# Kernel optimization log

Measured on AMD Instinct MI355X. Metric: run time of the kernel, lower is better.

Reference implementation:

```python
import jax, jax.numpy as jnp
import numpy as np

B, T, I, H = 64, 512, 512, 512

def setup_inputs() -> dict:
    key = jax.random.key(0)
    ks = jax.random.split(key, 13)
    s = 0.02
    return {
        'inputs': jax.random.normal(ks[0], (B, T, I), dtype=jnp.float32),
        'W_i': jax.random.normal(ks[1], (I, H), dtype=jnp.float32) * s,
        'W_f': jax.random.normal(ks[2], (I, H), dtype=jnp.float32) * s,
        'W_o': jax.random.normal(ks[3], (I, H), dtype=jnp.float32) * s,
        'W_c': jax.random.normal(ks[4], (I, H), dtype=jnp.float32) * s,
        'U_i': jax.random.normal(ks[5], (H, H), dtype=jnp.float32) * s,
        'U_f': jax.random.normal(ks[6], (H, H), dtype=jnp.float32) * s,
        'U_o': jax.random.normal(ks[7], (H, H), dtype=jnp.float32) * s,
        'U_c': jax.random.normal(ks[8], (H, H), dtype=jnp.float32) * s,
        'b_i': jax.random.normal(ks[9], (1, H), dtype=jnp.float32) * s,
        'b_f': jax.random.normal(ks[10], (1, H), dtype=jnp.float32) * s,
        'b_o': jax.random.normal(ks[11], (1, H), dtype=jnp.float32) * s,
        'b_c': jax.random.normal(ks[12], (1, H), dtype=jnp.float32) * s,
    }

def reference(inputs, W_i, W_f, W_o, W_c, U_i, U_f, U_o, U_c, b_i, b_f, b_o, b_c):
    batch = inputs.shape[0]
    hidden = U_i.shape[0]
    # Precompute input projections for all 4 gates in one fused GEMM: [T, B, 4H]
    W = jnp.concatenate([W_i, W_f, W_o, W_c], axis=1)          # [I, 4H]
    b = jnp.concatenate([b_i, b_f, b_o, b_c], axis=1)          # [1, 4H]
    U = jnp.concatenate([U_i, U_f, U_o, U_c], axis=1)          # [H, 4H]
    x_proj = jnp.einsum('bti,ig->tbg', inputs, W) + b          # [T, B, 4H]

    def step(carry, xg):
        h, c = carry
        g = xg + h @ U                                          # [B, 4H]
        i_g = jax.nn.sigmoid(g[:, 0*hidden:1*hidden])
        f_g = jax.nn.sigmoid(g[:, 1*hidden:2*hidden])
        o_g = jax.nn.sigmoid(g[:, 2*hidden:3*hidden])
        c_t = jnp.tanh(g[:, 3*hidden:4*hidden])
        c = f_g * c + i_g * c_t
        h = o_g * jnp.tanh(c)
        return (h, c), None

    h0 = jnp.zeros((batch, hidden), dtype=inputs.dtype)
    c0 = jnp.zeros((batch, hidden), dtype=inputs.dtype)
    (h, c), _ = jax.lax.scan(step, (h0, c0), x_proj)
    return h
```

## Files before the change

kernel.cpp:

```cpp
#include <hip/hip_runtime.h>
#include <hip/hip_bf16.h>
#include <cstdint>


typedef __bf16 bf16;
typedef __bf16 bf16x8 __attribute__((ext_vector_type(8)));
typedef float floatx4 __attribute__((ext_vector_type(4)));
typedef uint64_t u64;
typedef uint32_t u32;

#define T_STEPS 512

#define XP_OFF     0ull
#define XBF_OFF    134217728ull
#define WCT_OFF    167772160ull
#define USW_OFF    169869312ull
#define BCAT_OFF   171966464ull
#define HBUF_OFF   171974656ull

__device__ inline u32 pack_bf16x2(float a, float b) {
    union { __bf16 h[2]; u32 u; } cv;
    cv.h[0] = (__bf16)a; cv.h[1] = (__bf16)b;
    return cv.u;
}
__device__ inline float bf_lo(u32 w) { return __builtin_bit_cast(float, w << 16); }
__device__ inline float bf_hi(u32 w) { return __builtin_bit_cast(float, w & 0xffff0000u); }

__global__ void k0a_convert(const float* __restrict__ in, bf16* __restrict__ xbf) {
    int o = blockIdx.x * 256 + threadIdx.x;
    int k = o & 511;
    int r = o >> 9;
    int t = r >> 6, b = r & 63;
    xbf[o] = (bf16)in[(b * 512 + t) * 512 + k];
}

__global__ void k0b_wcat(const float* __restrict__ Wi, const float* __restrict__ Wf,
                         const float* __restrict__ Wo, const float* __restrict__ Wc,
                         const float* __restrict__ bi, const float* __restrict__ bfv,
                         const float* __restrict__ bo, const float* __restrict__ bc,
                         bf16* __restrict__ wct, float* __restrict__ bcat) {
    int o = blockIdx.x * 256 + threadIdx.x;
    int k = o & 511;
    int c = o >> 9;
    int h = c >> 2, g = c & 3;
    const float* W = (g == 0) ? Wi : (g == 1) ? Wf : (g == 2) ? Wo : Wc;
    wct[o] = (bf16)W[k * 512 + h];
    if (o < 2048) {
        int hh = o >> 2, gg = o & 3;
        const float* bv = (gg == 0) ? bi : (gg == 1) ? bfv : (gg == 2) ? bo : bc;
        bcat[o] = bv[hh];
    }
}

__global__ void k0c_uswz(const float* __restrict__ Ui, const float* __restrict__ Uf,
                         const float* __restrict__ Uo, const float* __restrict__ Uc,
                         bf16* __restrict__ usw) {
    int o = blockIdx.x * 256 + threadIdx.x;
    int e  = o & 7;
    int l  = (o >> 3) & 63;
    int ks = (o >> 9) & 15;
    int nt = (o >> 13) & 1;
    int w  = (o >> 14) & 3;
    int s  = o >> 16;
    int k = ks * 32 + (l >> 4) * 8 + e;
    int col_local = (2 * w + nt) * 16 + (l & 15);
    int h = s * 32 + (col_local >> 2);
    int g = col_local & 3;
    const float* U = (g == 0) ? Ui : (g == 1) ? Uf : (g == 2) ? Uo : Uc;
    usw[o] = (bf16)U[k * 512 + h];
}

__launch_bounds__(256, 2)
__global__ void k1_gemm(const bf16* __restrict__ xbf, const bf16* __restrict__ wct,
                        const float* __restrict__ bcat, bf16* __restrict__ xp) {
    __shared__ bf16 As[128 * 40];
    __shared__ bf16 Bs[128 * 40];
    int tid = threadIdx.x;
    int wid = tid >> 6, lane = tid & 63;
    int q = lane >> 4, m = lane & 15;
    int wr = wid >> 1, wc = wid & 1;
    int br = blockIdx.x & 255, bc = blockIdx.x >> 8;

    floatx4 acc[4][4] = {};

    for (int kk = 0; kk < 16; ++kk) {
        #pragma unroll
        for (int cc = 0; cc < 2; ++cc) {
            int ch = tid + cc * 256;
            int row = ch >> 2, part = ch & 3;
            bf16x8 va = *(const bf16x8*)&xbf[(br * 128 + row) * 512 + kk * 32 + part * 8];
            bf16x8 vb = *(const bf16x8*)&wct[(bc * 128 + row) * 512 + kk * 32 + part * 8];
            *(bf16x8*)&As[row * 40 + part * 8] = va;
            *(bf16x8*)&Bs[row * 40 + part * 8] = vb;
        }
        __syncthreads();
        bf16x8 af[4], bfr[4];
        #pragma unroll
        for (int i = 0; i < 4; ++i) {
            af[i]  = *(const bf16x8*)&As[(wr * 64 + i * 16 + m) * 40 + q * 8];
            bfr[i] = *(const bf16x8*)&Bs[(wc * 64 + i * 16 + m) * 40 + q * 8];
        }
        #pragma unroll
        for (int mt = 0; mt < 4; ++mt)
            #pragma unroll
            for (int nt = 0; nt < 4; ++nt)
                acc[mt][nt] = __builtin_amdgcn_mfma_f32_16x16x32_bf16(
                    af[mt], bfr[nt], acc[mt][nt], 0, 0, 0);
        __syncthreads();
    }
    float bias[4];
    #pragma unroll
    for (int nt = 0; nt < 4; ++nt) bias[nt] = bcat[bc * 128 + wc * 64 + nt * 16 + m];
    #pragma unroll
    for (int mt = 0; mt < 4; ++mt) {
        #pragma unroll
        for (int nt = 0; nt < 4; ++nt) {
            u32 p0 = pack_bf16x2(acc[mt][nt][0] + bias[nt], acc[mt][nt][1] + bias[nt]);
            u32 p1 = pack_bf16x2(acc[mt][nt][2] + bias[nt], acc[mt][nt][3] + bias[nt]);
            size_t idx = (((((size_t)(br * 2 + wr) * 4 + mt) * 16 + bc) * 8
                           + wc * 4 + nt) * 64 + lane) * 4;
            uint2 v; v.x = p0; v.y = p1;
            *(uint2*)&xp[idx] = v;
        }
    }
}

__launch_bounds__(256, 1)
__global__ void k2_rec(const bf16* __restrict__ xp, const bf16* __restrict__ usw,
                       u64* __restrict__ hbuf, float* __restrict__ out) {
    __shared__ bf16 h_lds[16 * 544];
    u32* h32 = (u32*)h_lds;

    int tid = threadIdx.x;
    int wid = tid >> 6, lane = tid & 63;
    int q = lane >> 4, m = lane & 15;
    int v = m >> 2, a = m & 3;
    int bg = blockIdx.x & 3, s = blockIdx.x >> 2;

    bf16x8 bfr[2][16];
    {
        const bf16x8* base = (const bf16x8*)usw;
        #pragma unroll
        for (int nt = 0; nt < 2; ++nt)
            #pragma unroll
            for (int ks = 0; ks < 16; ++ks)
                bfr[nt][ks] = base[(((s * 4 + wid) * 2 + nt) * 16 + ks) * 64 + lane];
    }

    int ra = q * 4 + a;
    float cs0 = 0.f, cs1 = 0.f;
    int pc_local = 4 * wid + 2 * (v & 1) + (v >> 1);
    int u0 = 8 * wid + v, u1 = 8 * wid + 4 + v;

    for (int t = 0; t < T_STEPS; ++t) {
        uint2 vx0, vx1;
        {
            size_t b0 = (((((size_t)t * 4 + bg) * 16 + s) * 8 + wid * 2 + 0) * 64 + lane) * 4;
            size_t b1 = (((((size_t)t * 4 + bg) * 16 + s) * 8 + wid * 2 + 1) * 64 + lane) * 4;
            vx0 = *(const uint2*)&xp[b0];
            vx1 = *(const uint2*)&xp[b1];
        }

        floatx4 acc[2] = {};

        if (t > 0) {
            const u64* rb = hbuf + ((size_t)((t - 1) & 1) * 4 + bg) * 4096;
            u32 tg = (u32)t;
            u64 w[16];
            #pragma unroll
            for (int i = 0; i < 16; ++i)
                w[i] = __hip_atomic_load(rb + tid + 256 * i, __ATOMIC_RELAXED,
                                         __HIP_MEMORY_SCOPE_AGENT);
            while (true) {
                bool ok = true;
                #pragma unroll
                for (int i = 0; i < 16; ++i) ok &= ((u32)(w[i] >> 32) == tg);
                if (ok) break;
                #pragma unroll
                for (int i = 0; i < 16; ++i)
                    w[i] = __hip_atomic_load(rb + tid + 256 * i, __ATOMIC_RELAXED,
                                             __HIP_MEMORY_SCOPE_AGENT);
            }
            #pragma unroll
            for (int i = 0; i < 16; ++i)
                h32[i * 272 + tid] = (u32)w[i];
            __syncthreads();
            #pragma unroll
            for (int ks = 0; ks < 16; ++ks) {
                bf16x8 af = *(const bf16x8*)&h_lds[m * 544 + ks * 32 + q * 8];
                acc[0] = __builtin_amdgcn_mfma_f32_16x16x32_bf16(af, bfr[0][ks], acc[0], 0, 0, 0);
                acc[1] = __builtin_amdgcn_mfma_f32_16x16x32_bf16(af, bfr[1][ks], acc[1], 0, 0, 0);
            }
        }

        acc[0][0] += bf_lo(vx0.x); acc[0][1] += bf_hi(vx0.x);
        acc[0][2] += bf_lo(vx0.y); acc[0][3] += bf_hi(vx0.y);
        acc[1][0] += bf_lo(vx1.x); acc[1][1] += bf_hi(vx1.x);
        acc[1][2] += bf_lo(vx1.y); acc[1][3] += bf_hi(vx1.y);

        float h0, h1;
        #pragma unroll
        for (int nt = 0; nt < 2; ++nt) {
            float x0 = acc[nt][0], x1 = acc[nt][1], x2 = acc[nt][2], x3 = acc[nt][3];
            {
                int a0 = a & 1;
                float p0 = a0 ? x0 : x1;
                float p1 = a0 ? x2 : x3;
                float r0 = __shfl_xor(p0, 1, 64);
                float r1 = __shfl_xor(p1, 1, 64);
                x0 = a0 ? r0 : x0;  x1 = a0 ? x1 : r0;
                x2 = a0 ? r1 : x2;  x3 = a0 ? x3 : r1;
            }
            {
                int a1 = (a >> 1) & 1;
                float p0 = a1 ? x0 : x2;
                float p1 = a1 ? x1 : x3;
                float r0 = __shfl_xor(p0, 2, 64);
                float r1 = __shfl_xor(p1, 2, 64);
                x0 = a1 ? r0 : x0;  x2 = a1 ? x2 : r0;
                x1 = a1 ? r1 : x1;  x3 = a1 ? x3 : r1;
            }
            float ig = 1.f / (1.f + __expf(-x0));
            float fg = 1.f / (1.f + __expf(-x1));
            float og = 1.f / (1.f + __expf(-x2));
            float th = 1.f - 2.f / (__expf(2.f * x3) + 1.f);
            float& cs = nt ? cs1 : cs0;
            cs = fg * cs + ig * th;
            float hv = og * (1.f - 2.f / (__expf(2.f * cs) + 1.f));
            if (nt) h1 = hv; else h0 = hv;
        }

        float hx0 = __shfl_xor(h0, 4, 64);
        float hx1 = __shfl_xor(h1, 4, 64);
        float he = (v & 1) ? hx1 : h0;
        float ho = (v & 1) ? h1  : hx0;
        u64 word = ((u64)(u32)(t + 1) << 32) | (u64)pack_bf16x2(he, ho);
        __hip_atomic_store(hbuf + ((((size_t)(t & 1) * 4 + bg) * 16 + ra) * 256)
                                + s * 16 + pc_local,
                           word, __ATOMIC_RELAXED, __HIP_MEMORY_SCOPE_AGENT);
        if (t == T_STEPS - 1) {
            out[(bg * 16 + ra) * 512 + s * 32 + u0] = h0;
            out[(bg * 16 + ra) * 512 + s * 32 + u1] = h1;
        }
    }
}

extern "C" void kernel_launch(void* const* d_in, const int* in_sizes, int n_in,
                              void* d_out, int out_size, void* d_ws, size_t ws_size,
                              hipStream_t stream) {
    const float* inp = (const float*)d_in[0];
    const float* Wi  = (const float*)d_in[1];
    const float* Wf  = (const float*)d_in[2];
    const float* Wo  = (const float*)d_in[3];
    const float* Wc  = (const float*)d_in[4];
    const float* Ui  = (const float*)d_in[5];
    const float* Uf  = (const float*)d_in[6];
    const float* Uo  = (const float*)d_in[7];
    const float* Uc  = (const float*)d_in[8];
    const float* bi  = (const float*)d_in[9];
    const float* bfv = (const float*)d_in[10];
    const float* bo  = (const float*)d_in[11];
    const float* bc  = (const float*)d_in[12];

    char* ws = (char*)d_ws;
    bf16*  xp    = (bf16*)(ws + XP_OFF);
    bf16*  xbf   = (bf16*)(ws + XBF_OFF);
    bf16*  wct   = (bf16*)(ws + WCT_OFF);
    bf16*  usw   = (bf16*)(ws + USW_OFF);
    float* bcat  = (float*)(ws + BCAT_OFF);
    u64*   hbuf  = (u64*)(ws + HBUF_OFF);

    k0a_convert<<<65536, 256, 0, stream>>>(inp, xbf);
    k0b_wcat<<<4096, 256, 0, stream>>>(Wi, Wf, Wo, Wc, bi, bfv, bo, bc, wct, bcat);
    k0c_uswz<<<4096, 256, 0, stream>>>(Ui, Uf, Uo, Uc, usw);
    k1_gemm<<<4096, 256, 0, stream>>>(xbf, wct, bcat, xp);
    k2_rec<<<64, 256, 0, stream>>>(xp, usw, hbuf, (float*)d_out);
}
```

Before: 1.723 ms.

## Prefetch next-step projections, coalesce h exchange stores, use lightweight LDS barrier

Loads the next timestep's input projection during the current step and seeds the accumulator with it, so the MFMA chain no longer waits on a global load. The h exchange buffer is re-laid out so each block writes a contiguous slice and the reader scatters words into a repadded LDS tile (row stride 520). The barrier now waits only on LDS counters, and a short s_sleep is added before polling the flags. This targets per-step latency in the serial recurrence but risks LDS bank conflicts and extra polling delay from the sleep.

```diff
diff --git a/kernel.cpp b/kernel.cpp
--- a/kernel.cpp
+++ b/kernel.cpp
@@ -25,6 +25,13 @@
 }
 __device__ inline float bf_lo(u32 w) { return __builtin_bit_cast(float, w << 16); }
 __device__ inline float bf_hi(u32 w) { return __builtin_bit_cast(float, w & 0xffff0000u); }
+
+__device__ inline void lgkm_barrier() {
+    __atomic_signal_fence(__ATOMIC_SEQ_CST);
+    __builtin_amdgcn_s_waitcnt(0xc07f);
+    __builtin_amdgcn_s_barrier();
+    __atomic_signal_fence(__ATOMIC_SEQ_CST);
+}
 
 __global__ void k0a_convert(const float* __restrict__ in, bf16* __restrict__ xbf) {
     int o = blockIdx.x * 256 + threadIdx.x;
@@ -128,7 +135,7 @@
 __launch_bounds__(256, 1)
 __global__ void k2_rec(const bf16* __restrict__ xp, const bf16* __restrict__ usw,
                        u64* __restrict__ hbuf, float* __restrict__ out) {
-    __shared__ bf16 h_lds[16 * 544];
+    __shared__ bf16 h_lds[16 * 520];
     u32* h32 = (u32*)h_lds;
 
     int tid = threadIdx.x;
@@ -148,22 +155,32 @@
     }
 
     int ra = q * 4 + a;
+    int P = 4 * wid + 2 * (v & 1) + (v >> 1);
+    int u0 = 8 * wid + v, u1 = 8 * wid + 4 + v;
     float cs0 = 0.f, cs1 = 0.f;
-    int pc_local = 4 * wid + 2 * (v & 1) + (v >> 1);
-    int u0 = 8 * wid + v, u1 = 8 * wid + 4 + v;
+
+    int stage_base = ra * 260 + P;
+
+    uint2 vx0, vx1;
+    {
+        size_t b0 = ((((size_t)bg * 16 + s) * 8 + wid * 2) * 64 + lane) * 4;
+        vx0 = *(const uint2*)&xp[b0];
+        vx1 = *(const uint2*)&xp[b0 + 256];
+    }
 
     for (int t = 0; t < T_STEPS; ++t) {
-        uint2 vx0, vx1;
-        {
-            size_t b0 = (((((size_t)t * 4 + bg) * 16 + s) * 8 + wid * 2 + 0) * 64 + lane) * 4;
-            size_t b1 = (((((size_t)t * 4 + bg) * 16 + s) * 8 + wid * 2 + 1) * 64 + lane) * 4;
-            vx0 = *(const uint2*)&xp[b0];
-            vx1 = *(const uint2*)&xp[b1];
-        }
-
-        floatx4 acc[2] = {};
+        floatx4 acc[2];
+
+        acc[0][0] = bf_lo(vx0.x); acc[0][1] = bf_hi(vx0.x);
+        acc[0][2] = bf_lo(vx0.y); acc[0][3] = bf_hi(vx0.y);
+        acc[1][0] = bf_lo(vx1.x); acc[1][1] = bf_hi(vx1.x);
+        acc[1][2] = bf_lo(vx1.y); acc[1][3] = bf_hi(vx1.y);
 
         if (t > 0) {
+            __atomic_signal_fence(__ATOMIC_SEQ_CST);
+            __builtin_amdgcn_s_sleep(8);
+            __atomic_signal_fence(__ATOMIC_SEQ_CST);
+
             const u64* rb = hbuf + ((size_t)((t - 1) & 1) * 4 + bg) * 4096;
             u32 tg = (u32)t;
             u64 w[16];
@@ -171,7 +188,7 @@
             for (int i = 0; i < 16; ++i)
                 w[i] = __hip_atomic_load(rb + tid + 256 * i, __ATOMIC_RELAXED,
                                          __HIP_MEMORY_SCOPE_AGENT);
-            while (true) {
+            for (;;) {
                 bool ok = true;
                 #pragma unroll
                 for (int i = 0; i < 16; ++i) ok &= ((u32)(w[i] >> 32) == tg);
@@ -183,20 +200,21 @@
             }
             #pragma unroll
             for (int i = 0; i < 16; ++i)
-                h32[i * 272 + tid] = (u32)w[i];
-            __syncthreads();
+                h32[stage_base + i * 16] = (u32)w[i];
+            lgkm_barrier();
             #pragma unroll
             for (int ks = 0; ks < 16; ++ks) {
-                bf16x8 af = *(const bf16x8*)&h_lds[m * 544 + ks * 32 + q * 8];
+                bf16x8 af = *(const bf16x8*)&h_lds[m * 520 + ks * 32 + q * 8];
                 acc[0] = __builtin_amdgcn_mfma_f32_16x16x32_bf16(af, bfr[0][ks], acc[0], 0, 0, 0);
                 acc[1] = __builtin_amdgcn_mfma_f32_16x16x32_bf16(af, bfr[1][ks], acc[1], 0, 0, 0);
             }
         }
 
-        acc[0][0] += bf_lo(vx0.x); acc[0][1] += bf_hi(vx0.x);
-        acc[0][2] += bf_lo(vx0.y); acc[0][3] += bf_hi(vx0.y);
-        acc[1][0] += bf_lo(vx1.x); acc[1][1] += bf_hi(vx1.x);
-        acc[1][2] += bf_lo(vx1.y); acc[1][3] += bf_hi(vx1.y);
+        if (t + 1 < T_STEPS) {
+            size_t b0 = (((((size_t)(t + 1) * 4 + bg) * 16 + s) * 8 + wid * 2) * 64 + lane) * 4;
+            vx0 = *(const uint2*)&xp[b0];
+            vx1 = *(const uint2*)&xp[b0 + 256];
+        }
 
         float h0, h1;
         #pragma unroll
@@ -235,8 +253,8 @@
         float he = (v & 1) ? hx1 : h0;
         float ho = (v & 1) ? h1  : hx0;
         u64 word = ((u64)(u32)(t + 1) << 32) | (u64)pack_bf16x2(he, ho);
-        __hip_atomic_store(hbuf + ((((size_t)(t & 1) * 4 + bg) * 16 + ra) * 256)
-                                + s * 16 + pc_local,
+        __hip_atomic_store(hbuf + ((size_t)(t & 1) * 4 + bg) * 4096
+                                + s * 256 + wid * 64 + lane,
                            word, __ATOMIC_RELAXED, __HIP_MEMORY_SCOPE_AGENT);
         if (t == T_STEPS - 1) {
             out[(bg * 16 + ra) * 512 + s * 32 + u0] = h0;
```

Measured after the change: 1.464 ms. 15.0% less time.
